# Performance work log

Measured on AMD Instinct MI355X. Metric: run time of the kernel, lower is better.

Reference implementation:

```python
import jax, jax.numpy as jnp
import numpy as np

SEQ, B, IN, H, L = 2048, 64, 512, 512, 2

def _xavier(key, shape):
    fan_out, fan_in = shape
    bound = float(np.sqrt(6.0 / (fan_in + fan_out)))
    return jax.random.uniform(key, shape, jnp.float32, -bound, bound)

def setup_inputs() -> dict:
    key = jax.random.key(0)
    ks = jax.random.split(key, 5)
    x = jax.random.normal(ks[0], (SEQ, B, IN), jnp.float32)
    # layer 0: input_size=IN; layer 1: input_size=H. Biases init to zeros (reset_parameters).
    return {
        "x": x,
        "W_ih0": _xavier(ks[1], (H, IN)),
        "W_hh0": _xavier(ks[2], (H, H)),
        "b_ih0": jnp.zeros((H,), jnp.float32),
        "b_hh0": jnp.zeros((H,), jnp.float32),
        "W_ih1": _xavier(ks[3], (H, H)),
        "W_hh1": _xavier(ks[4], (H, H)),
        "b_ih1": jnp.zeros((H,), jnp.float32),
        "b_hh1": jnp.zeros((H,), jnp.float32),
    }

def _run_layer(x_in, W_ih, W_hh, b_ih, b_hh):
    # Precompute input projection for all timesteps (matches forward_optimized / same math as forward).
    proj = jnp.einsum('sbi,hi->sbh', x_in, W_ih) + b_ih  # [S,B,H]
    h0 = jnp.zeros((x_in.shape[1], W_hh.shape[0]), x_in.dtype)
    def step(h, p_t):
        h_new = jnp.tanh(p_t + h @ W_hh.T + b_hh)
        return h_new, h_new
    h_final, outs = jax.lax.scan(step, h0, proj)
    return outs, h_final

def reference(x, W_ih0, W_hh0, b_ih0, b_hh0, W_ih1, W_hh1, b_ih1, b_hh1):
    out0, h0 = _run_layer(x, W_ih0, W_hh0, b_ih0, b_hh0)
    out1, h1 = _run_layer(out0, W_ih1, W_hh1, b_ih1, b_hh1)
    hidden = jnp.stack([h0, h1], axis=0)  # [num_layers, B, H]
    return out1, hidden
```

## Files before the change

kernel.cpp:

```cpp
#include <hip/hip_runtime.h>
#include <cstdint>
#include <cstddef>

#define SEQ   2048
#define BATCH 64
#define HID   512

__global__ __launch_bounds__(256)
void proj_gemm(const float* __restrict__ A, const float* __restrict__ W,
               const float* __restrict__ bias, float* __restrict__ C)
{
    __shared__ float As[16][132];
    __shared__ float Bs[16][132];
    const int t  = threadIdx.x;
    const int bm = blockIdx.x >> 2;
    const int bn = blockIdx.x & 3;
    const int m0 = bm * 128;
    const int n0 = bn * 128;
    const int tn = t & 15;
    const int tm = t >> 4;

    float acc[8][8];
#pragma unroll
    for (int i = 0; i < 8; ++i)
#pragma unroll
        for (int j = 0; j < 8; ++j) acc[i][j] = 0.f;

    const int lrow = t >> 2;
    const int lk4  = t & 3;

    for (int kk = 0; kk < 512; kk += 16) {
#pragma unroll
        for (int i = 0; i < 2; ++i) {
            const int row = lrow + i * 64;
            float4 va = *(const float4*)&A[(size_t)(m0 + row) * 512 + kk + lk4 * 4];
            As[lk4 * 4 + 0][row] = va.x;
            As[lk4 * 4 + 1][row] = va.y;
            As[lk4 * 4 + 2][row] = va.z;
            As[lk4 * 4 + 3][row] = va.w;
            float4 vb = *(const float4*)&W[(size_t)(n0 + row) * 512 + kk + lk4 * 4];
            Bs[lk4 * 4 + 0][row] = vb.x;
            Bs[lk4 * 4 + 1][row] = vb.y;
            Bs[lk4 * 4 + 2][row] = vb.z;
            Bs[lk4 * 4 + 3][row] = vb.w;
        }
        __syncthreads();
#pragma unroll
        for (int k = 0; k < 16; ++k) {
            float4 a0 = *(const float4*)&As[k][tm * 8];
            float4 a1 = *(const float4*)&As[k][tm * 8 + 4];
            float4 b0 = *(const float4*)&Bs[k][tn * 4];
            float4 b1 = *(const float4*)&Bs[k][64 + tn * 4];
            float ar[8] = {a0.x, a0.y, a0.z, a0.w, a1.x, a1.y, a1.z, a1.w};
            float bc[8] = {b0.x, b0.y, b0.z, b0.w, b1.x, b1.y, b1.z, b1.w};
#pragma unroll
            for (int i = 0; i < 8; ++i)
#pragma unroll
                for (int j = 0; j < 8; ++j)
                    acc[i][j] = fmaf(ar[i], bc[j], acc[i][j]);
        }
        __syncthreads();
    }

    float4 bv0 = *(const float4*)&bias[n0 + tn * 4];
    float4 bv1 = *(const float4*)&bias[n0 + 64 + tn * 4];
    const float bb[8] = {bv0.x, bv0.y, bv0.z, bv0.w, bv1.x, bv1.y, bv1.z, bv1.w};
#pragma unroll
    for (int i = 0; i < 8; ++i) {
        const size_t rowoff = (size_t)(m0 + tm * 8 + i) * 512 + n0;
        float4 o0, o1;
        o0.x = acc[i][0] + bb[0]; o0.y = acc[i][1] + bb[1];
        o0.z = acc[i][2] + bb[2]; o0.w = acc[i][3] + bb[3];
        o1.x = acc[i][4] + bb[4]; o1.y = acc[i][5] + bb[5];
        o1.z = acc[i][6] + bb[6]; o1.w = acc[i][7] + bb[7];
        *(float4*)&C[rowoff + tn * 4] = o0;
        *(float4*)&C[rowoff + 64 + tn * 4] = o1;
    }
}

__device__ __forceinline__ float fast_tanh(float x)
{
    const float e = __builtin_amdgcn_exp2f(x * 2.88539008177793f);
    return fmaf(-2.0f, __builtin_amdgcn_rcpf(e + 1.0f), 1.0f);
}

__global__ __launch_bounds__(512, 2)
void rnn_scan(const float* __restrict__ proj, const float* __restrict__ Whh,
              const float* __restrict__ bhh, float* __restrict__ out,
              float* __restrict__ hidden, unsigned long long* __restrict__ hbuf)
{
    extern __shared__ float lds[];
    float4* Wv4 = (float4*)lds;
    float4* hS4 = (float4*)(lds + 32768);
    float*  hSf = lds + 32768;

    const int t    = threadIdx.x;
    const int bid  = blockIdx.x;
    const int g    = bid & 31;
    const int s    = bid >> 5;
    const int b0   = g * 2;
    const int base = s * 64;
    const int w    = t >> 6;
    const int l    = t & 63;
    const int rr   = l & 7;
    const int kc   = l >> 3;
    const int row  = base + w * 8 + rr;

    const float4* Wg4 = (const float4*)Whh;
    {
        const int k0 = kc * 16;
#pragma unroll
        for (int j = 0; j < 16; ++j)
            Wv4[w * 1024 + j * 64 + l] = Wg4[(size_t)row * 128 + k0 + j];
    }
    const bool pub  = (kc < 2);
    const float breg = pub ? bhh[row] : 0.f;

    for (int i = t; i < 2176; i += 512) hSf[i] = 0.f;
    __syncthreads();

    const bool own  = (t >= base) && (t < base + 64);
    const int  pado = (t >> 6) * 68 + (t & 63);

    float pv_next = 0.f;
    if (pub) pv_next = proj[(size_t)(b0 + kc) * HID + row];

    unsigned long long* gb = hbuf + (size_t)g * 4096;

    for (int step = 0; step < SEQ; ++step) {
        const int p = step & 1;

        const float pv = pv_next;
        if (pub && step + 1 < SEQ)
            pv_next = proj[((size_t)(step + 1) * BATCH + (b0 + kc)) * HID + row];

        if (!own) {
            const unsigned int want = (unsigned int)step;
            const unsigned long long* f0 = gb + (size_t)p * 2048 + t;
            const unsigned long long* f1 = f0 + 512;
            unsigned long long x0 = 0, x1 = 0;
            bool ok0 = false, ok1 = false;
            int spins = 0;
            for (;;) {
                if (!ok0) {
                    x0 = __hip_atomic_load(f0, __ATOMIC_RELAXED, __HIP_MEMORY_SCOPE_AGENT);
                    ok0 = (unsigned int)(x0 >> 32) == want;
                }
                if (!ok1) {
                    x1 = __hip_atomic_load(f1, __ATOMIC_RELAXED, __HIP_MEMORY_SCOPE_AGENT);
                    ok1 = (unsigned int)(x1 >> 32) == want;
                }
                if (ok0 & ok1) break;
                __builtin_amdgcn_s_sleep(1);
                if (++spins > 4096) {
                    __builtin_amdgcn_fence(__ATOMIC_ACQUIRE, "agent");
                    spins = 0;
                }
            }
            hSf[p * 1088 + pado]       = __uint_as_float((unsigned int)x0);
            hSf[p * 1088 + 544 + pado] = __uint_as_float((unsigned int)x1);
        }
        __syncthreads();

        const float4* wb = Wv4 + w * 1024 + l;
        const float4* h0 = hS4 + p * 272 + kc * 17;
        const float4* h1 = h0 + 136;
        float a0e = 0.f, a0o = 0.f, a1e = 0.f, a1o = 0.f;
#pragma unroll
        for (int j = 0; j < 16; j += 2) {
            float4 wa = wb[j * 64];
            float4 wc = wb[(j + 1) * 64];
            float4 p0 = h0[j], p1 = h0[j + 1];
            float4 q0 = h1[j], q1 = h1[j + 1];
            a0e = fmaf(wa.x, p0.x, a0e); a0e = fmaf(wa.y, p0.y, a0e);
            a0e = fmaf(wa.z, p0.z, a0e); a0e = fmaf(wa.w, p0.w, a0e);
            a1e = fmaf(wa.x, q0.x, a1e); a1e = fmaf(wa.y, q0.y, a1e);
            a1e = fmaf(wa.z, q0.z, a1e); a1e = fmaf(wa.w, q0.w, a1e);
            a0o = fmaf(wc.x, p1.x, a0o); a0o = fmaf(wc.y, p1.y, a0o);
            a0o = fmaf(wc.z, p1.z, a0o); a0o = fmaf(wc.w, p1.w, a0o);
            a1o = fmaf(wc.x, q1.x, a1o); a1o = fmaf(wc.y, q1.y, a1o);
            a1o = fmaf(wc.z, q1.z, a1o); a1o = fmaf(wc.w, q1.w, a1o);
        }
        float s0 = a0e + a0o;
        float s1 = a1e + a1o;
        s0 += __shfl_xor(s0, 8, 64);  s1 += __shfl_xor(s1, 8, 64);
        s0 += __shfl_xor(s0, 16, 64); s1 += __shfl_xor(s1, 16, 64);
        s0 += __shfl_xor(s0, 32, 64); s1 += __shfl_xor(s1, 32, 64);

        if (pub) {
            const float sum = (kc == 0) ? s0 : s1;
            const int   bb  = b0 + kc;
            const float hn  = fast_tanh(pv + breg + sum);
            out[((size_t)step * BATCH + bb) * HID + row] = hn;
            const unsigned long long pk =
                ((unsigned long long)(unsigned int)(step + 1) << 32) |
                (unsigned long long)__float_as_uint(hn);
            __hip_atomic_store(gb + (size_t)(p ^ 1) * 2048 + (size_t)kc * 512 + row,
                               pk, __ATOMIC_RELAXED, __HIP_MEMORY_SCOPE_AGENT);
            hSf[(p ^ 1) * 1088 + kc * 544 + (row >> 6) * 68 + (row & 63)] = hn;
            if (step == SEQ - 1) hidden[(size_t)bb * HID + row] = hn;
        }
    }
}

extern "C" void kernel_launch(void* const* d_in, const int* in_sizes, int n_in,
                              void* d_out, int out_size, void* d_ws, size_t ws_size,
                              hipStream_t stream)
{
    (void)in_sizes; (void)n_in; (void)out_size; (void)ws_size;

    const float* x    = (const float*)d_in[0];
    const float* Wih0 = (const float*)d_in[1];
    const float* Whh0 = (const float*)d_in[2];
    const float* bih0 = (const float*)d_in[3];
    const float* bhh0 = (const float*)d_in[4];
    const float* Wih1 = (const float*)d_in[5];
    const float* Whh1 = (const float*)d_in[6];
    const float* bih1 = (const float*)d_in[7];
    const float* bhh1 = (const float*)d_in[8];

    float* out1   = (float*)d_out;
    float* hidden = out1 + (size_t)SEQ * BATCH * HID;

    float* proj = (float*)d_ws;
    unsigned long long* hbufA = (unsigned long long*)(proj + (size_t)SEQ * BATCH * HID);
    unsigned long long* hbufB = hbufA + (size_t)32 * 4096;

    hipMemsetAsync(hbufA, 0, (size_t)2 * 32 * 4096 * sizeof(unsigned long long),
                   stream);

    const size_t shmem = (size_t)(32768 + 2176) * sizeof(float);
    (void)hipFuncSetAttribute((const void*)rnn_scan,
                              hipFuncAttributeMaxDynamicSharedMemorySize, (int)shmem);

    proj_gemm<<<dim3(4096), dim3(256), 0, stream>>>(x, Wih0, bih0, proj);
    {
        const float* p = proj; const float* w = Whh0; const float* bb = bhh0;
        float* o = out1; float* hd = hidden; unsigned long long* hb = hbufA;
        void* args[] = {&p, &w, &bb, &o, &hd, &hb};
        hipLaunchCooperativeKernel((const void*)rnn_scan, dim3(256), dim3(512),
                                   args, (unsigned)shmem, stream);
    }

    proj_gemm<<<dim3(4096), dim3(256), 0, stream>>>(out1, Wih1, bih1, proj);
    {
        const float* p = proj; const float* w = Whh1; const float* bb = bhh1;
        float* o = out1; float* hd = hidden + BATCH * HID; unsigned long long* hb = hbufB;
        void* args[] = {&p, &w, &bb, &o, &hd, &hb};
        hipLaunchCooperativeKernel((const void*)rnn_scan, dim3(256), dim3(512),
                                   args, (unsigned)shmem, stream);
    }
}
```

Measured before the change: 9.655 ms.

## Interleave two batch-pair phases per block to hide cross-block sync latency

Each block now owns 32 hidden rows across 4 batch elements, split into two independent pairs processed in alternating phases. While one pair computes its matvec, the block's global-flag poll for the other pair is already in flight, so the spin-wait latency overlaps with compute. The grid becomes 16 groups by 16 slices, with a smaller W slice per block and the h buffers indexed by pair and parity. In exchange, each block does more serial work per step and there are twice as many barriers per timestep.

Result: slower. 13.91 ms (+44.1%).

```diff
diff --git a/kernel.cpp b/kernel.cpp
--- a/kernel.cpp
+++ b/kernel.cpp
@@ -90,116 +90,120 @@
               float* __restrict__ hidden, unsigned long long* __restrict__ hbuf)
 {
     extern __shared__ float lds[];
-    float4* Wv4 = (float4*)lds;
-    float4* hS4 = (float4*)(lds + 32768);
-    float*  hSf = lds + 32768;
+    float4* WL  = (float4*)lds;
+    float4* hL4 = (float4*)(lds + 16384);
+    float*  hLf = lds + 16384;
 
     const int t    = threadIdx.x;
     const int bid  = blockIdx.x;
-    const int g    = bid & 31;
-    const int s    = bid >> 5;
-    const int b0   = g * 2;
-    const int base = s * 64;
-    const int w    = t >> 6;
-    const int l    = t & 63;
-    const int rr   = l & 7;
-    const int kc   = l >> 3;
-    const int row  = base + w * 8 + rr;
-
-    const float4* Wg4 = (const float4*)Whh;
-    {
-        const int k0 = kc * 16;
-#pragma unroll
-        for (int j = 0; j < 16; ++j)
-            Wv4[w * 1024 + j * 64 + l] = Wg4[(size_t)row * 128 + k0 + j];
-    }
+    const int g    = bid & 15;
+    const int s    = bid >> 4;
+    const int base = s * 32;
+    const int rl   = t >> 4;
+    const int kc   = t & 15;
+    const int row  = base + rl;
+    const int e00  = g * 4;
+
+    const float4* W4 = (const float4*)Whh;
+#pragma unroll
+    for (int j = 0; j < 8; ++j)
+        WL[j * 512 + t] = W4[(size_t)row * 128 + kc * 8 + j];
+
     const bool pub  = (kc < 2);
     const float breg = pub ? bhh[row] : 0.f;
 
-    for (int i = t; i < 2176; i += 512) hSf[i] = 0.f;
+    for (int i = t; i < 4608; i += 512) hLf[i] = 0.f;
     __syncthreads();
 
-    const bool own  = (t >= base) && (t < base + 64);
-    const int  pado = (t >> 6) * 68 + (t & 63);
-
-    float pv_next = 0.f;
-    if (pub) pv_next = proj[(size_t)(b0 + kc) * HID + row];
-
+    const bool own = (t >= base) && (t < base + 32);
     unsigned long long* gb = hbuf + (size_t)g * 4096;
 
-    for (int step = 0; step < SEQ; ++step) {
-        const int p = step & 1;
-
-        const float pv = pv_next;
-        if (pub && step + 1 < SEQ)
-            pv_next = proj[((size_t)(step + 1) * BATCH + (b0 + kc)) * HID + row];
-
-        if (!own) {
-            const unsigned int want = (unsigned int)step;
-            const unsigned long long* f0 = gb + (size_t)p * 2048 + t;
-            const unsigned long long* f1 = f0 + 512;
-            unsigned long long x0 = 0, x1 = 0;
-            bool ok0 = false, ok1 = false;
+    float pv0 = 0.f, pv1 = 0.f;
+    if (pub) {
+        pv0 = proj[(size_t)(e00 + 0 + kc) * HID + row];
+        pv1 = proj[(size_t)(e00 + 2 + kc) * HID + row];
+    }
+
+    auto phase = [&](const int P, const int S, float& pv) {
+        const int Pn = P ^ 1;
+        const int Sn = S + P;
+        const int pr = S & 1;
+        const bool dopoll = (!own) && (Sn < SEQ);
+
+        unsigned long long x0 = 0, x1 = 0;
+        unsigned long long* pb = gb + (size_t)Pn * 2048 + (size_t)(Sn & 1) * 1024;
+        if (dopoll) {
+            x0 = __hip_atomic_load(pb + t,       __ATOMIC_RELAXED, __HIP_MEMORY_SCOPE_AGENT);
+            x1 = __hip_atomic_load(pb + 512 + t, __ATOMIC_RELAXED, __HIP_MEMORY_SCOPE_AGENT);
+        }
+
+        const float4* ha = hL4 + ((size_t)(P * 2 + pr) * 2 + 0) * 144 + kc * 9;
+        const float4* hb = ha + 144;
+        const float4* wb = WL + t;
+        float A0 = 0.f, B0 = 0.f, A1 = 0.f, B1 = 0.f;
+#pragma unroll
+        for (int j = 0; j < 8; j += 2) {
+            float4 w0 = wb[j * 512];
+            float4 w1 = wb[(j + 1) * 512];
+            float4 p0 = ha[j], p1 = ha[j + 1];
+            float4 q0 = hb[j], q1 = hb[j + 1];
+            A0 = fmaf(w0.x, p0.x, A0); A0 = fmaf(w0.y, p0.y, A0);
+            A0 = fmaf(w0.z, p0.z, A0); A0 = fmaf(w0.w, p0.w, A0);
+            B0 = fmaf(w0.x, q0.x, B0); B0 = fmaf(w0.y, q0.y, B0);
+            B0 = fmaf(w0.z, q0.z, B0); B0 = fmaf(w0.w, q0.w, B0);
+            A1 = fmaf(w1.x, p1.x, A1); A1 = fmaf(w1.y, p1.y, A1);
+            A1 = fmaf(w1.z, p1.z, A1); A1 = fmaf(w1.w, p1.w, A1);
+            B1 = fmaf(w1.x, q1.x, B1); B1 = fmaf(w1.y, q1.y, B1);
+            B1 = fmaf(w1.z, q1.z, B1); B1 = fmaf(w1.w, q1.w, B1);
+        }
+        float t0 = A0 + A1, t1 = B0 + B1;
+        t0 += __shfl_xor(t0, 1, 64); t1 += __shfl_xor(t1, 1, 64);
+        t0 += __shfl_xor(t0, 2, 64); t1 += __shfl_xor(t1, 2, 64);
+        t0 += __shfl_xor(t0, 4, 64); t1 += __shfl_xor(t1, 4, 64);
+        t0 += __shfl_xor(t0, 8, 64); t1 += __shfl_xor(t1, 8, 64);
+
+        if (pub) {
+            const int elem = e00 + P * 2 + kc;
+            const float sum = (kc == 0) ? t0 : t1;
+            const float hn = fast_tanh(pv + breg + sum);
+            out[((size_t)S * BATCH + elem) * HID + row] = hn;
+            const unsigned long long pk =
+                ((unsigned long long)(unsigned)(S + 1) << 32) |
+                (unsigned long long)__float_as_uint(hn);
+            __hip_atomic_store(gb + (size_t)P * 2048 + (size_t)((S + 1) & 1) * 1024
+                               + (size_t)kc * 512 + row,
+                               pk, __ATOMIC_RELAXED, __HIP_MEMORY_SCOPE_AGENT);
+            hLf[((size_t)(P * 2 + ((S + 1) & 1)) * 2 + kc) * 576
+                + (row >> 5) * 36 + (row & 31)] = hn;
+            if (S == SEQ - 1) hidden[(size_t)elem * HID + row] = hn;
+            if (S + 1 < SEQ)
+                pv = proj[((size_t)(S + 1) * BATCH + elem) * HID + row];
+        }
+
+        if (dopoll) {
+            const unsigned want = (unsigned)Sn;
             int spins = 0;
-            for (;;) {
-                if (!ok0) {
-                    x0 = __hip_atomic_load(f0, __ATOMIC_RELAXED, __HIP_MEMORY_SCOPE_AGENT);
-                    ok0 = (unsigned int)(x0 >> 32) == want;
-                }
-                if (!ok1) {
-                    x1 = __hip_atomic_load(f1, __ATOMIC_RELAXED, __HIP_MEMORY_SCOPE_AGENT);
-                    ok1 = (unsigned int)(x1 >> 32) == want;
-                }
-                if (ok0 & ok1) break;
+            while (((unsigned)(x0 >> 32) != want) | ((unsigned)(x1 >> 32) != want)) {
                 __builtin_amdgcn_s_sleep(1);
+                if ((unsigned)(x0 >> 32) != want)
+                    x0 = __hip_atomic_load(pb + t, __ATOMIC_RELAXED, __HIP_MEMORY_SCOPE_AGENT);
+                if ((unsigned)(x1 >> 32) != want)
+                    x1 = __hip_atomic_load(pb + 512 + t, __ATOMIC_RELAXED, __HIP_MEMORY_SCOPE_AGENT);
                 if (++spins > 4096) {
                     __builtin_amdgcn_fence(__ATOMIC_ACQUIRE, "agent");
                     spins = 0;
                 }
             }
-            hSf[p * 1088 + pado]       = __uint_as_float((unsigned int)x0);
-            hSf[p * 1088 + 544 + pado] = __uint_as_float((unsigned int)x1);
+            const int hfb = ((Pn * 2 + (Sn & 1)) * 2) * 576 + (t >> 5) * 36 + (t & 31);
+            hLf[hfb]       = __uint_as_float((unsigned)x0);
+            hLf[hfb + 576] = __uint_as_float((unsigned)x1);
         }
         __syncthreads();
-
-        const float4* wb = Wv4 + w * 1024 + l;
-        const float4* h0 = hS4 + p * 272 + kc * 17;
-        const float4* h1 = h0 + 136;
-        float a0e = 0.f, a0o = 0.f, a1e = 0.f, a1o = 0.f;
-#pragma unroll
-        for (int j = 0; j < 16; j += 2) {
-            float4 wa = wb[j * 64];
-            float4 wc = wb[(j + 1) * 64];
-            float4 p0 = h0[j], p1 = h0[j + 1];
-            float4 q0 = h1[j], q1 = h1[j + 1];
-            a0e = fmaf(wa.x, p0.x, a0e); a0e = fmaf(wa.y, p0.y, a0e);
-            a0e = fmaf(wa.z, p0.z, a0e); a0e = fmaf(wa.w, p0.w, a0e);
-            a1e = fmaf(wa.x, q0.x, a1e); a1e = fmaf(wa.y, q0.y, a1e);
-            a1e = fmaf(wa.z, q0.z, a1e); a1e = fmaf(wa.w, q0.w, a1e);
-            a0o = fmaf(wc.x, p1.x, a0o); a0o = fmaf(wc.y, p1.y, a0o);
-            a0o = fmaf(wc.z, p1.z, a0o); a0o = fmaf(wc.w, p1.w, a0o);
-            a1o = fmaf(wc.x, q1.x, a1o); a1o = fmaf(wc.y, q1.y, a1o);
-            a1o = fmaf(wc.z, q1.z, a1o); a1o = fmaf(wc.w, q1.w, a1o);
-        }
-        float s0 = a0e + a0o;
-        float s1 = a1e + a1o;
-        s0 += __shfl_xor(s0, 8, 64);  s1 += __shfl_xor(s1, 8, 64);
-        s0 += __shfl_xor(s0, 16, 64); s1 += __shfl_xor(s1, 16, 64);
-        s0 += __shfl_xor(s0, 32, 64); s1 += __shfl_xor(s1, 32, 64);
-
-        if (pub) {
-            const float sum = (kc == 0) ? s0 : s1;
-            const int   bb  = b0 + kc;
-            const float hn  = fast_tanh(pv + breg + sum);
-            out[((size_t)step * BATCH + bb) * HID + row] = hn;
-            const unsigned long long pk =
-                ((unsigned long long)(unsigned int)(step + 1) << 32) |
-                (unsigned long long)__float_as_uint(hn);
-            __hip_atomic_store(gb + (size_t)(p ^ 1) * 2048 + (size_t)kc * 512 + row,
-                               pk, __ATOMIC_RELAXED, __HIP_MEMORY_SCOPE_AGENT);
-            hSf[(p ^ 1) * 1088 + kc * 544 + (row >> 6) * 68 + (row & 63)] = hn;
-            if (step == SEQ - 1) hidden[(size_t)bb * HID + row] = hn;
-        }
+    };
+
+    for (int S = 0; S < SEQ; ++S) {
+        phase(0, S, pv0);
+        phase(1, S, pv1);
     }
 }
 
@@ -224,12 +228,12 @@
 
     float* proj = (float*)d_ws;
     unsigned long long* hbufA = (unsigned long long*)(proj + (size_t)SEQ * BATCH * HID);
-    unsigned long long* hbufB = hbufA + (size_t)32 * 4096;
-
-    hipMemsetAsync(hbufA, 0, (size_t)2 * 32 * 4096 * sizeof(unsigned long long),
+    unsigned long long* hbufB = hbufA + (size_t)16 * 4096;
+
+    hipMemsetAsync(hbufA, 0, (size_t)2 * 16 * 4096 * sizeof(unsigned long long),
                    stream);
 
-    const size_t shmem = (size_t)(32768 + 2176) * sizeof(float);
+    const size_t shmem = (size_t)(16384 + 4608) * sizeof(float);
     (void)hipFuncSetAttribute((const void*)rnn_scan,
                               hipFuncAttributeMaxDynamicSharedMemorySize, (int)shmem);
 
```
